# Performance work log

Hardware: AMD Instinct MI355X
Metric: run time of the kernel (lower is better)

## Reference

```python
import jax, jax.numpy as jnp
import numpy as np

T, N, NN = 16, 64, 32          # ob_T, agents, neighbors
D, H, DK, DFF, L = 512, 8, 64, 2048, 2
NUM_PRED, OB_R = 20, 2.0


def _w(k, shape):
    fan_in = shape[-2] if len(shape) > 1 else shape[-1]
    return jax.random.normal(k, shape, jnp.float32) / np.sqrt(fan_in).astype(np.float32)


def setup_inputs():
    key = jax.random.key(0)
    ks = jax.random.split(key, 16)
    return {
        "x": jax.random.normal(ks[0], (T, N, 6), jnp.float32),
        "neighbor": jax.random.normal(ks[1], (T, N, NN, 4), jnp.float32),
        "att_factor": jax.random.uniform(ks[2], (1,), jnp.float32),
        "Wx": _w(ks[3], (4, D)), "bx": jnp.zeros((D,), jnp.float32),
        "Wn": _w(ks[4], (3, D)), "bn": jnp.zeros((D,), jnp.float32),
        "Wpred": _w(ks[5], (D, 2)), "bpred": jnp.zeros((2,), jnp.float32),
        "WQ": _w(ks[6], (L, D, H * DK)),
        "WK": _w(ks[7], (L, D, H * DK)),
        "WV": _w(ks[8], (L, D, H * DK)),
        "Wfc": _w(ks[9], (L, H * DK, D)),
        "mha_ln_g": jnp.ones((L, D), jnp.float32), "mha_ln_b": jnp.zeros((L, D), jnp.float32),
        "WSI": _w(ks[10], (L, H * D, D)),
        "ffs_w1": _w(ks[11], (L, D, DFF)), "ffs_w2": _w(ks[12], (L, DFF, D)),
        "ffs_ln_g": jnp.ones((L, D), jnp.float32), "ffs_ln_b": jnp.zeros((L, D), jnp.float32),
        "ffi_w1": _w(ks[13], (L, D, DFF)), "ffi_w2": _w(ks[14], (L, DFF, D)),
        "ffi_ln_g": jnp.ones((L, D), jnp.float32), "ffi_ln_b": jnp.zeros((L, D), jnp.float32),
    }


def _ln(x, g, b, eps=1e-5):
    m = x.mean(-1, keepdims=True)
    v = x.var(-1, keepdims=True)
    return (x - m) / jnp.sqrt(v + eps) * g + b


def reference(x, neighbor, att_factor, Wx, bx, Wn, bn, Wpred, bpred,
              WQ, WK, WV, Wfc, mha_ln_g, mha_ln_b, WSI,
              ffs_w1, ffs_w2, ffs_ln_g, ffs_ln_b,
              ffi_w1, ffi_w2, ffi_ln_g, ffi_ln_b):
    # ---- trajectory features ----
    velocity = jnp.linalg.norm(x[:, :, 2:4], axis=-1, keepdims=True)
    v_angle = jnp.arctan(x[:, :, 5] / x[:, :, 4])[..., None]
    x_f = jnp.nan_to_num(jnp.concatenate([x[:, :, 0:2], velocity, v_angle], axis=-1))
    pos = x[..., :2]                                       # [T,N,2]
    v = jnp.concatenate([x[1:2, ..., 2:4], pos[1:] - pos[:-1]], axis=0)  # [T,N,2]
    dp = neighbor[..., :2] - pos[:, :, None, :]            # [T,N,Nn,2]
    dv = neighbor[..., 2:4] - v[:, :, None, :]
    dist = jnp.linalg.norm(dp, axis=-1)                    # [T,N,Nn]
    mask = (dist <= OB_R).transpose(1, 2, 0)               # [N,Nn,T] (query-time mask)
    dot_dp_v = jnp.einsum('tnmd,tnd->tnm', dp, v)
    bearing = dot_dp_v / (dist * jnp.linalg.norm(v, axis=-1)[:, :, None])
    bearing = jnp.where(jnp.isnan(bearing), 0.0, bearing)
    dot_dp_dv = jnp.einsum('tnmd,tnmd->tnm', dp, dv)
    tau = -dot_dp_dv / jnp.linalg.norm(dv, axis=-1)
    tau = jnp.clip(jnp.where(jnp.isnan(tau), 0.0, tau), 0.0, 7.0)
    mpd = jnp.linalg.norm(dp + tau[..., None] * dv, axis=-1)
    neighbor_f = jnp.nan_to_num(jnp.stack([dist, bearing, mpd], axis=-1))  # [T,N,Nn,3]

    # ---- positional encoding (note: pos * 10000^(2i/d), as in the source) ----
    position = jnp.arange(T, dtype=jnp.float32)[:, None]
    div = jnp.power(10000.0, jnp.arange(0, D, 2, dtype=jnp.float32) / D)
    pe = jnp.zeros((T, D), jnp.float32)
    pe = pe.at[:, 0::2].set(jnp.sin(position * div)).at[:, 1::2].set(jnp.cos(position * div))

    x_emb = (x_f @ Wx + bx) + pe[:, None, :]               # [T,N,D]
    n_emb = (neighbor_f @ Wn + bn) + pe[:, None, None, :]  # [T,N,Nn,D]
    x_emb = x_emb.transpose(1, 0, 2)                       # [N,T,D]
    n_emb = n_emb.transpose(1, 2, 0, 3)                    # [N,Nn,T,D]

    amask = mask[:, :, None, :, None]   # [N,Nn,1(heads),T(query),1(key)]
    factor = att_factor[0]
    sk = 1.0 / np.sqrt(DK).astype(np.float32)
    sd = 1.0 / np.sqrt(D).astype(np.float32)

    for l in range(L):
        # --- masked MHA over the time axis, per (agent, neighbor) ---
        q = (n_emb @ WQ[l]).reshape(N, NN, T, H, DK).transpose(0, 1, 3, 2, 4)
        k = (n_emb @ WK[l]).reshape(N, NN, T, H, DK).transpose(0, 1, 3, 2, 4)
        vv = (n_emb @ WV[l]).reshape(N, NN, T, H, DK).transpose(0, 1, 3, 2, 4)
        scores = jnp.einsum('bmhqd,bmhkd->bmhqk', q, k) * sk
        scores = jnp.where(amask, scores, -1e9)
        attn = jax.nn.softmax(scores, axis=-1)             # [N,Nn,H,T,T]
        ctx = jnp.einsum('bmhqk,bmhkd->bmhqd', attn, vv)
        ctx = ctx.transpose(0, 1, 3, 2, 4).reshape(N, NN, T, H * DK)
        res_inter = _ln(ctx @ Wfc[l] + n_emb, mha_ln_g[l], mha_ln_b[l])

        # --- self/inter attention fusion ---
        att_inter = attn.mean(axis=1)                      # [N,H,T,T]
        att_self = jax.nn.softmax(jnp.einsum('nqd,nkd->nqk', x_emb, x_emb) * sd, axis=-1)
        att = att_self[:, None, :, :] + factor * att_inter # [N,H,T,T]
        si = jnp.einsum('nhqt,ntd->nqhd', att, x_emb).reshape(N, T, H * D)
        x_new = si @ WSI[l]                                # [N,T,D]

        # --- FFN + LayerNorm (self and inter branches) ---
        x_emb = _ln(jax.nn.relu(x_new @ ffs_w1[l]) @ ffs_w2[l] + x_new,
                    ffs_ln_g[l], ffs_ln_b[l])
        n_emb = _ln(jax.nn.relu(res_inter @ ffi_w1[l]) @ ffi_w2[l] + res_inter,
                    ffi_ln_g[l], ffi_ln_b[l])

    out = x_emb @ Wpred + bpred                            # [N,T,2]
    out = jnp.broadcast_to(out[None], (NUM_PRED, N, T, 2)).transpose(0, 2, 1, 3)
    return out                                             # [20,T,N,2]
```

## Files before the change

### kernel.cpp

```cpp
#include <hip/hip_runtime.h>
#include <math.h>


#define T_ 16
#define N_ 64
#define NN_ 32
#define D_ 512
#define H_ 8
#define DK_ 64
#define DFF_ 2048
#define L_ 2
#define NPRED_ 20

typedef unsigned short u16;
typedef unsigned int u32;
typedef __attribute__((ext_vector_type(8))) short short8;
typedef __attribute__((ext_vector_type(4))) float f32x4;

__device__ __forceinline__ u16 f2bf(float f) {
    u32 u = __float_as_uint(f);
    u32 r = u + 0x7fffu + ((u >> 16) & 1u);
    return (u16)(r >> 16);
}
__device__ __forceinline__ float bfv(u16 v) {
    return __uint_as_float(((u32)v) << 16);
}
__device__ __forceinline__ float ntn(float v) {
    if (isnan(v)) return 0.0f;
    if (isinf(v)) return v > 0.0f ? 3.4028234663852886e38f : -3.4028234663852886e38f;
    return v;
}
__device__ __forceinline__ float wave_sum(float v) {
    #pragma unroll
    for (int o = 32; o > 0; o >>= 1) v += __shfl_xor(v, o, 64);
    return v;
}
__device__ __forceinline__ void gload_lds(const u16* g, u16* l) {
    __builtin_amdgcn_global_load_lds(
        (const __attribute__((address_space(1))) u32*)g,
        (__attribute__((address_space(3))) u32*)l, 16, 0, 0);
}

struct WJob { const float* src; u16* dst; int K; int N; int t0; };
struct WJobs { WJob j[14]; };
__global__ __launch_bounds__(256) void wconv_all(WJobs jobs, int ntiles) {
    int bid = blockIdx.x;
    if (bid >= ntiles) return;
    int ji = 0;
    #pragma unroll 1
    for (int i = 1; i < 14; ++i) if (bid >= jobs.j[i].t0) ji = i;
    const float* in = jobs.j[ji].src;
    u16* out = jobs.j[ji].dst;
    int K = jobs.j[ji].K, N = jobs.j[ji].N;
    int lt = bid - jobs.j[ji].t0;
    int ntx = N >> 5;
    int nb = (lt % ntx) * 32, kb = (lt / ntx) * 32;
    __shared__ float tile[32][33];
    int tx = threadIdx.x & 31, ty = threadIdx.x >> 5;
    #pragma unroll
    for (int r = ty; r < 32; r += 8)
        tile[r][tx] = in[(size_t)(kb + r) * N + nb + tx];
    __syncthreads();
    #pragma unroll
    for (int r = ty; r < 32; r += 8)
        out[(size_t)(nb + r) * K + kb + tx] = f2bf(tile[tx][r]);
}

template<int TM, int TN, int EPI, int WF32, int WBF16>
__global__ __launch_bounds__(256) void gemm_bt(
    const u16* __restrict__ Ab, const u16* __restrict__ Btb,
    float* __restrict__ Cf, u16* __restrict__ Cb, const void* __restrict__ Rg,
    int K, int ldc)
{
    constexpr int WR = TM / 32, WC = TN / 32;
    constexpr int ITA = TM / 32, ITB = TN / 32;
    __shared__ __align__(16) u16 As[TM][64];
    __shared__ __align__(16) u16 Bs[TN][64];
    int tid = threadIdx.x;
    int lane = tid & 63, wave = tid >> 6;
    int quad = lane >> 4, l16 = lane & 15;
    int wm = (wave >> 1) * (TM / 2), wn = (wave & 1) * (TN / 2);

    int gx = gridDim.x, gy = gridDim.y;
    int bx, by;
    if ((gy & 7) == 0) {
        int id = blockIdx.y * gx + blockIdx.x;
        int xcd = id & 7;
        int slot = id >> 3;
        bx = slot % gx;
        by = xcd * (gy >> 3) + slot / gx;
    } else {
        bx = blockIdx.x;
        by = blockIdx.y;
    }
    size_t row0 = (size_t)by * TM;
    size_t col0 = (size_t)bx * TN;

    f32x4 acc[WR][WC];
    #pragma unroll
    for (int i = 0; i < WR; ++i)
        #pragma unroll
        for (int j = 0; j < WC; ++j)
            acc[i][j] = (f32x4){0.f, 0.f, 0.f, 0.f};

    int srow = lane >> 3;
    int c8 = (lane & 7) ^ srow;
    int h8 = l16 & 7;

    for (int k0 = 0; k0 < K; k0 += 64) {
        __syncthreads();
        #pragma unroll
        for (int it = 0; it < ITA; ++it) {
            int g = wave + it * 4;
            gload_lds(Ab + (row0 + g * 8 + srow) * (size_t)K + k0 + c8 * 8, &As[g * 8][0]);
        }
        #pragma unroll
        for (int it = 0; it < ITB; ++it) {
            int g = wave + it * 4;
            gload_lds(Btb + (col0 + g * 8 + srow) * (size_t)K + k0 + c8 * 8, &Bs[g * 8][0]);
        }
        __syncthreads();
        #pragma unroll
        for (int s = 0; s < 2; ++s) {
            int coff = ((s * 4 + quad) ^ h8) * 8;
            short8 af[WR], bf[WC];
            #pragma unroll
            for (int i = 0; i < WR; ++i)
                af[i] = *(short8*)&As[wm + i * 16 + l16][coff];
            #pragma unroll
            for (int j = 0; j < WC; ++j)
                bf[j] = *(short8*)&Bs[wn + j * 16 + l16][coff];
            #pragma unroll
            for (int i = 0; i < WR; ++i)
                #pragma unroll
                for (int j = 0; j < WC; ++j)
                    acc[i][j] = __builtin_amdgcn_mfma_f32_16x16x32_bf16(
                        af[i], bf[j], acc[i][j], 0, 0, 0);
        }
    }
    #pragma unroll
    for (int i = 0; i < WR; ++i)
        #pragma unroll
        for (int j = 0; j < WC; ++j)
            #pragma unroll
            for (int reg = 0; reg < 4; ++reg) {
                size_t row = row0 + wm + i * 16 + quad * 4 + reg;
                size_t col = col0 + wn + j * 16 + l16;
                float v = acc[i][j][reg];
                if (EPI == 2) v += ((const float*)Rg)[row * (size_t)ldc + col];
                if (EPI == 3) v += bfv(((const u16*)Rg)[row * (size_t)ldc + col]);
                if (EPI == 1) v = fmaxf(v, 0.f);
                if (WF32)  Cf[row * (size_t)ldc + col] = v;
                if (WBF16) Cb[row * (size_t)ldc + col] = f2bf(v);
            }
}

template<int TM, int TN, int WMW, int WNW, int EPI, int WF32, int WBF16>
__global__ __launch_bounds__(WMW * WNW * 64, 2) void gemm_pp(
    const u16* __restrict__ Ab, const u16* __restrict__ Btb,
    float* __restrict__ Cf, u16* __restrict__ Cb, const void* __restrict__ Rg,
    int K, int ldc)
{
    constexpr int NW = WMW * WNW;
    constexpr int FM = TM / WMW / 16;
    constexpr int FN = TN / WNW / 16;
    constexpr int MH = (FM * FN > 16) ? 2 : 1;
    constexpr int FMp = FM / MH;
    constexpr int GA = TM / 8 / NW;
    constexpr int GB = TN / 8 / NW;
    __shared__ __align__(16) u16 As[2][TM][64];
    __shared__ __align__(16) u16 Bs[2][TN][64];
    int tid = threadIdx.x;
    int lane = tid & 63, wave = tid >> 6;
    int quad = lane >> 4, l16 = lane & 15;
    int wm = (wave / WNW) * (FM * 16);
    int wn = (wave % WNW) * (FN * 16);

    int gx = gridDim.x, gy = gridDim.y;
    int bx, by;
    {
        int id = blockIdx.y * gx + blockIdx.x;
        int xcd = id & 7, slot = id >> 3;
        bx = slot % gx;
        by = xcd * (gy >> 3) + slot / gx;
    }
    size_t row0 = (size_t)by * TM;
    size_t col0 = (size_t)bx * TN;

    f32x4 acc[FM][FN];
    #pragma unroll
    for (int i = 0; i < FM; ++i)
        #pragma unroll
        for (int j = 0; j < FN; ++j)
            acc[i][j] = (f32x4){0.f, 0.f, 0.f, 0.f};

    int srow = lane >> 3;
    int c8 = (lane & 7) ^ srow;
    int h8 = l16 & 7;
    size_t aoff[GA], boff[GB];
    #pragma unroll
    for (int it = 0; it < GA; ++it)
        aoff[it] = (row0 + (size_t)(wave + it * NW) * 8 + srow) * (size_t)K + c8 * 8;
    #pragma unroll
    for (int it = 0; it < GB; ++it)
        boff[it] = (col0 + (size_t)(wave + it * NW) * 8 + srow) * (size_t)K + c8 * 8;

    int nt = K >> 6;
    #pragma unroll
    for (int it = 0; it < GA; ++it)
        gload_lds(Ab + aoff[it], &As[0][(wave + it * NW) * 8][0]);
    #pragma unroll
    for (int it = 0; it < GB; ++it)
        gload_lds(Btb + boff[it], &Bs[0][(wave + it * NW) * 8][0]);
    asm volatile("s_waitcnt vmcnt(0)" ::: "memory");
    __builtin_amdgcn_s_barrier();

    #pragma unroll 1
    for (int t = 0; t < nt; ++t) {
        int cur = t & 1;
        if (t + 1 < nt) {
            size_t ko = (size_t)(t + 1) * 64;
            #pragma unroll
            for (int it = 0; it < GA; ++it)
                gload_lds(Ab + aoff[it] + ko, &As[cur ^ 1][(wave + it * NW) * 8][0]);
            #pragma unroll
            for (int it = 0; it < GB; ++it)
                gload_lds(Btb + boff[it] + ko, &Bs[cur ^ 1][(wave + it * NW) * 8][0]);
        }
        short8 bf[FN];
        #pragma unroll
        for (int kh = 0; kh < 2; ++kh) {
            #pragma unroll
            for (int mh = 0; mh < MH; ++mh) {
                int coff = ((kh * 4 + quad) ^ h8) * 8;
                short8 af[FMp];
                if (mh == 0) {
                    #pragma unroll
                    for (int j = 0; j < FN; ++j)
                        bf[j] = *(short8*)&Bs[cur][wn + j * 16 + l16][coff];
                }
                #pragma unroll
                for (int i = 0; i < FMp; ++i)
                    af[i] = *(short8*)&As[cur][wm + (mh * FMp + i) * 16 + l16][coff];
                __builtin_amdgcn_s_barrier();
                __builtin_amdgcn_s_setprio(1);
                #pragma unroll
                for (int i = 0; i < FMp; ++i)
                    #pragma unroll
                    for (int j = 0; j < FN; ++j)
                        acc[mh * FMp + i][j] = __builtin_amdgcn_mfma_f32_16x16x32_bf16(
                            af[i], bf[j], acc[mh * FMp + i][j], 0, 0, 0);
                __builtin_amdgcn_s_setprio(0);
                __builtin_amdgcn_s_barrier();
            }
        }
        if (t + 1 < nt)
            asm volatile("s_waitcnt vmcnt(0)" ::: "memory");
        __builtin_amdgcn_s_barrier();
    }

    #pragma unroll
    for (int i = 0; i < FM; ++i)
        #pragma unroll
        for (int j = 0; j < FN; ++j)
            #pragma unroll
            for (int reg = 0; reg < 4; ++reg) {
                size_t row = row0 + wm + i * 16 + quad * 4 + reg;
                size_t col = col0 + wn + j * 16 + l16;
                float v = acc[i][j][reg];
                if (EPI == 2) v += ((const float*)Rg)[row * (size_t)ldc + col];
                if (EPI == 3) v += bfv(((const u16*)Rg)[row * (size_t)ldc + col]);
                if (EPI == 1) v = fmaxf(v, 0.f);
                if (WF32)  Cf[row * (size_t)ldc + col] = v;
                if (WBF16) Cb[row * (size_t)ldc + col] = f2bf(v);
            }
}

template<int CTX, int LD>
__global__ __launch_bounds__(256) void attn_fused_kernel(
    const u16* __restrict__ QKVb, const float* __restrict__ maskf, int bm0,
    float* __restrict__ att_sum, u16* __restrict__ ctxb)
{
    __shared__ __align__(16) u16 sQ[16][520];
    __shared__ __align__(16) u16 sK[16][520];
    __shared__ __align__(16) u16 sV[CTX ? 16 : 1][520];
    __shared__ float s_p[H_][16][17];
    int bm_l = blockIdx.x;
    int tid = threadIdx.x;
    int t = tid >> 4, ch = (tid & 15) * 32;
    const u16* base = QKVb + ((size_t)bm_l * T_ + t) * LD;
    #pragma unroll
    for (int c = 0; c < 4; ++c) {
        *(uint4*)&sQ[t][ch + c * 8] = *(const uint4*)(base + ch + c * 8);
        *(uint4*)&sK[t][ch + c * 8] = *(const uint4*)(base + 512 + ch + c * 8);
        if (CTX) *(uint4*)&sV[t][ch + c * 8] = *(const uint4*)(base + 1024 + ch + c * 8);
    }
    __syncthreads();

    int b = (bm0 + bm_l) >> 5;

    #pragma unroll
    for (int r = 0; r < 8; ++r) {
        int h = r;
        int q = (tid >> 4) & 15, k = tid & 15;
        const u32* qu = (const u32*)&sQ[q][0] + h * 32;
        const u32* ku = (const u32*)&sK[k][0] + h * 32;
        float acc = 0.f;
        #pragma unroll
        for (int j = 0; j < 32; ++j) {
            u32 a = qu[j], bb = ku[j];
            acc += bfv((u16)(a & 0xffff)) * bfv((u16)(bb & 0xffff));
            acc += bfv((u16)(a >> 16))    * bfv((u16)(bb >> 16));
        }
        acc *= 0.125f;
        if (maskf[(size_t)(bm0 + bm_l) * T_ + q] == 0.0f) acc = -1e9f;
        s_p[h][q][k] = acc;
    }
    __syncthreads();
    if (tid < 128) {
        int h = tid >> 4, q = tid & 15;
        float mx = -3.4e38f;
        #pragma unroll
        for (int kk = 0; kk < 16; ++kk) mx = fmaxf(mx, s_p[h][q][kk]);
        float e[16], s = 0.f;
        #pragma unroll
        for (int kk = 0; kk < 16; ++kk) { e[kk] = expf(s_p[h][q][kk] - mx); s += e[kk]; }
        float inv = 1.0f / s;
        #pragma unroll
        for (int kk = 0; kk < 16; ++kk) s_p[h][q][kk] = e[kk] * inv;
    }
    __syncthreads();
    #pragma unroll
    for (int r = 0; r < 8; ++r) {
        int h = r;
        int q = (tid >> 4) & 15, k = tid & 15;
        atomicAdd(&att_sum[(((size_t)b * H_ + h) * T_ + q) * T_ + k], s_p[h][q][k]);
    }
    if (CTX) {
        #pragma unroll
        for (int rep = 0; rep < 16; ++rep) {
            int i2 = rep * 256 + tid;
            int tt = i2 >> 8, c2 = i2 & 255;
            int h = c2 >> 5;
            const float* pr = &s_p[h][tt][0];
            float a0 = 0.f, a1 = 0.f;
            #pragma unroll
            for (int kk = 0; kk < 16; ++kk) {
                u32 vv = *((const u32*)&sV[kk][0] + c2);
                float p = pr[kk];
                a0 += p * bfv((u16)(vv & 0xffff));
                a1 += p * bfv((u16)(vv >> 16));
            }
            u32 o = (u32)f2bf(a0) | ((u32)f2bf(a1) << 16);
            *((u32*)(ctxb + ((size_t)bm_l * T_ + tt) * D_) + c2) = o;
        }
    }
}

__global__ __launch_bounds__(256) void siatt_kernel(
    const float* __restrict__ xemb, const float* __restrict__ att_sum,
    const float* __restrict__ attf, u16* __restrict__ sib)
{
    __shared__ float sX[16][516];
    __shared__ float sS[16][17];
    __shared__ float sA[16][17];
    int n = blockIdx.x >> 3, h = blockIdx.x & 7;
    int tid = threadIdx.x;
    int t = tid >> 4, ch = (tid & 15) * 32;
    const float* src = xemb + ((size_t)n * T_ + t) * D_;
    #pragma unroll
    for (int c = 0; c < 8; ++c)
        *(float4*)&sX[t][ch + c * 4] = *(const float4*)(src + ch + c * 4);
    __syncthreads();
    int q = tid >> 4, k = tid & 15;
    {
        float acc = 0.f;
        for (int d = 0; d < D_; ++d) acc += sX[q][d] * sX[k][d];
        sS[q][k] = acc * 0.04419417382415922f;
    }
    __syncthreads();
    if (tid < T_) {
        float mx = -3.4e38f;
        #pragma unroll
        for (int kk = 0; kk < 16; ++kk) mx = fmaxf(mx, sS[tid][kk]);
        float e[16], s = 0.f;
        #pragma unroll
        for (int kk = 0; kk < 16; ++kk) { e[kk] = expf(sS[tid][kk] - mx); s += e[kk]; }
        float inv = 1.0f / s;
        #pragma unroll
        for (int kk = 0; kk < 16; ++kk) sS[tid][kk] = e[kk] * inv;
    }
    __syncthreads();
    float f = attf[0] * (1.0f / 32.0f);
    sA[q][k] = sS[q][k] + f * att_sum[((size_t)n * H_ + h) * 256 + q * 16 + k];
    __syncthreads();
    #pragma unroll
    for (int rep = 0; rep < 16; ++rep) {
        int i2 = rep * 256 + tid;
        int qq = i2 >> 8, d2 = (i2 & 255) * 2;
        const float* ar = &sA[qq][0];
        float a0 = 0.f, a1 = 0.f;
        #pragma unroll
        for (int tt = 0; tt < 16; ++tt) {
            float p = ar[tt];
            a0 += p * sX[tt][d2];
            a1 += p * sX[tt][d2 + 1];
        }
        u32 o = (u32)f2bf(a0) | ((u32)f2bf(a1) << 16);
        *((u32*)(sib + (size_t)n * T_ * 4096 + (size_t)qq * 4096 + h * 512) + (d2 >> 1)) = o;
    }
}

__global__ void pe_kernel(float* pe) {
    int i = blockIdx.x * blockDim.x + threadIdx.x;
    if (i >= T_ * 256) return;
    int t = i >> 8, j = i & 255;
    float dv = (float)pow(10000.0, (double)j / 256.0);
    float a = (float)t * dv;
    double ad = (double)a;
    pe[t * D_ + 2 * j]     = (float)sin(ad);
    pe[t * D_ + 2 * j + 1] = (float)cos(ad);
}

__global__ void xemb_kernel(const float* x, const float* Wx, const float* bx,
                            const float* pe, float* xemb) {
    int row = blockIdx.x;
    int t = row / N_, n = row % N_;
    float x0 = x[row * 6 + 0], x1 = x[row * 6 + 1];
    float x2 = x[row * 6 + 2], x3 = x[row * 6 + 3];
    float x4 = x[row * 6 + 4], x5 = x[row * 6 + 5];
    float vel = sqrtf(x2 * x2 + x3 * x3);
    float ang = atanf(x5 / x4);
    float f0 = ntn(x0), f1 = ntn(x1), f2 = ntn(vel), f3 = ntn(ang);
    for (int d = threadIdx.x; d < D_; d += blockDim.x) {
        xemb[((size_t)n * T_ + t) * D_ + d] =
            f0 * Wx[0 * D_ + d] + f1 * Wx[1 * D_ + d]
          + f2 * Wx[2 * D_ + d] + f3 * Wx[3 * D_ + d]
          + bx[d] + pe[t * D_ + d];
    }
}

__global__ void nbr_kernel(const float* x, const float* nbr, float* nf, float* maskf) {
    int idx = blockIdx.x * blockDim.x + threadIdx.x;
    if (idx >= T_ * N_ * NN_) return;
    int m = idx % NN_;
    int tn = idx / NN_;
    int n = tn % N_, t = tn / N_;
    float px = x[((size_t)t * N_ + n) * 6 + 0];
    float py = x[((size_t)t * N_ + n) * 6 + 1];
    float vx, vy;
    if (t == 0) {
        vx = x[((size_t)1 * N_ + n) * 6 + 2];
        vy = x[((size_t)1 * N_ + n) * 6 + 3];
    } else {
        vx = px - x[((size_t)(t - 1) * N_ + n) * 6 + 0];
        vy = py - x[((size_t)(t - 1) * N_ + n) * 6 + 1];
    }
    float nx  = nbr[(size_t)idx * 4 + 0], ny  = nbr[(size_t)idx * 4 + 1];
    float nvx = nbr[(size_t)idx * 4 + 2], nvy = nbr[(size_t)idx * 4 + 3];
    float dpx = nx - px, dpy = ny - py;
    float dvx = nvx - vx, dvy = nvy - vy;
    float dist = sqrtf(dpx * dpx + dpy * dpy);
    maskf[((size_t)n * NN_ + m) * T_ + t] = (dist <= 2.0f) ? 1.0f : 0.0f;
    float vn = sqrtf(vx * vx + vy * vy);
    float bearing = (dpx * vx + dpy * vy) / (dist * vn);
    if (isnan(bearing)) bearing = 0.0f;
    float dvn = sqrtf(dvx * dvx + dvy * dvy);
    float tau = -(dpx * dvx + dpy * dvy) / dvn;
    if (isnan(tau)) tau = 0.0f;
    tau = fminf(fmaxf(tau, 0.0f), 7.0f);
    float mx_ = dpx + tau * dvx, my_ = dpy + tau * dvy;
    float mpd = sqrtf(mx_ * mx_ + my_ * my_);
    nf[(size_t)idx * 3 + 0] = ntn(dist);
    nf[(size_t)idx * 3 + 1] = ntn(bearing);
    nf[(size_t)idx * 3 + 2] = ntn(mpd);
}

__global__ void nemb_kernel(const float* nf, const float* Wn, const float* bn,
                            const float* pe, u16* Ab) {
    int row = blockIdx.x;
    int t = row % T_;
    int bm = row / T_;
    int m = bm % NN_, b = bm / NN_;
    size_t nfrow = (((size_t)t * N_ + b) * NN_ + m) * 3;
    float f0 = nf[nfrow], f1 = nf[nfrow + 1], f2 = nf[nfrow + 2];
    for (int d = threadIdx.x; d < D_; d += blockDim.x) {
        float v = f0 * Wn[d] + f1 * Wn[D_ + d] + f2 * Wn[2 * D_ + d]
                + bn[d] + pe[t * D_ + d];
        Ab[(size_t)row * D_ + d] = f2bf(v);
    }
}

template<int INBF>
__global__ __launch_bounds__(256) void ln_kernel(
    const void* X, const float* g, const float* b, float* outF, u16* outB, int nrows) {
    int row = blockIdx.x * 4 + (threadIdx.x >> 6);
    if (row >= nrows) return;
    int lane = threadIdx.x & 63;
    float v[8];
    float s = 0.f;
    #pragma unroll
    for (int r = 0; r < 8; ++r) {
        int d = lane + r * 64;
        v[r] = INBF ? bfv(((const u16*)X)[(size_t)row * D_ + d])
                    : ((const float*)X)[(size_t)row * D_ + d];
        s += v[r];
    }
    s = wave_sum(s);
    float mean = s * (1.0f / 512.0f);
    float vs = 0.f;
    #pragma unroll
    for (int r = 0; r < 8; ++r) { float d = v[r] - mean; vs += d * d; }
    vs = wave_sum(vs);
    float rstd = rsqrtf(vs * (1.0f / 512.0f) + 1e-5f);
    #pragma unroll
    for (int r = 0; r < 8; ++r) {
        int d = lane + r * 64;
        float o = (v[r] - mean) * rstd * g[d] + b[d];
        if (outF) outF[(size_t)row * D_ + d] = o;
        if (outB) outB[(size_t)row * D_ + d] = f2bf(o);
    }
}

__global__ void predbcast_kernel(const float* xemb, const float* Wp, const float* bp,
                                 float* out) {
    int idx = blockIdx.x * blockDim.x + threadIdx.x;
    if (idx >= N_ * T_ * 2) return;
    int c = idx & 1;
    int nt = idx >> 1;
    int n = nt / T_, t = nt % T_;
    float acc = bp[c];
    for (int j = 0; j < D_; ++j) acc += xemb[(size_t)nt * D_ + j] * Wp[(size_t)j * 2 + c];
    #pragma unroll
    for (int p = 0; p < NPRED_; ++p)
        out[(((size_t)p * T_ + t) * N_ + n) * 2 + c] = acc;
}

extern "C" void kernel_launch(void* const* d_in, const int* in_sizes, int n_in,
                              void* d_out, int out_size, void* d_ws, size_t ws_size,
                              hipStream_t stream) {
    (void)in_sizes; (void)n_in; (void)out_size; (void)ws_size;

    const float* x    = (const float*)d_in[0];
    const float* nbr  = (const float*)d_in[1];
    const float* attf = (const float*)d_in[2];
    const float* Wx   = (const float*)d_in[3];
    const float* bx   = (const float*)d_in[4];
    const float* Wn   = (const float*)d_in[5];
    const float* bn   = (const float*)d_in[6];
    const float* Wp   = (const float*)d_in[7];
    const float* bp   = (const float*)d_in[8];
    const float* WQ   = (const float*)d_in[9];
    const float* WK   = (const float*)d_in[10];
    const float* WV   = (const float*)d_in[11];
    const float* Wfc  = (const float*)d_in[12];
    const float* mlng = (const float*)d_in[13];
    const float* mlnb = (const float*)d_in[14];
    const float* WSI  = (const float*)d_in[15];
    const float* fsw1 = (const float*)d_in[16];
    const float* fsw2 = (const float*)d_in[17];
    const float* fsg  = (const float*)d_in[18];
    const float* fsb  = (const float*)d_in[19];
    const float* fiw1 = (const float*)d_in[20];
    const float* fiw2 = (const float*)d_in[21];
    const float* fig  = (const float*)d_in[22];
    const float* fib  = (const float*)d_in[23];

    char* w = (char*)d_ws;
    size_t off = 0;
    auto alloc = [&](size_t bytes) -> void* {
        void* p = w + off;
        off = (off + bytes + 255) & ~(size_t)255;
        return p;
    };
    const size_t MiB = 1024 * 1024;

    const int BM = N_ * NN_;
    const int ROWS_I = BM * T_;
    const int CB = 1024;
    const int RC = CB * T_;
    const int NCH = ROWS_I / RC;

    float* pe      = (float*)alloc((size_t)T_ * D_ * 4);
    float* xemb    = (float*)alloc((size_t)N_ * T_ * D_ * 4);
    float* nf      = (float*)alloc((size_t)T_ * N_ * NN_ * 3 * 4);
    float* maskf   = (float*)alloc((size_t)BM * T_ * 4);
    u16*   Ab      = (u16*)alloc((size_t)ROWS_I * D_ * 2);
    u16* tQKV[2], *tWSI[2], *tfs1[2], *tfs2[2];
    for (int l = 0; l < 2; ++l) {
        tQKV[l] = (u16*)alloc((size_t)1536 * 512 * 2);
        tWSI[l] = (u16*)alloc((size_t)512 * 4096 * 2);
        tfs1[l] = (u16*)alloc((size_t)2048 * 512 * 2);
        tfs2[l] = (u16*)alloc((size_t)512 * 2048 * 2);
    }
    u16* tWfc = (u16*)alloc((size_t)512 * 512 * 2);
    u16* tfi1 = (u16*)alloc((size_t)2048 * 512 * 2);
    u16* tfi2 = (u16*)alloc((size_t)512 * 2048 * 2);
    char* SCR  = (char*)alloc(64 * MiB);
    u16*   QKVb = (u16*)SCR;
    u16*   ctxb = (u16*)(SCR + 48 * MiB);
    u16*   hid  = (u16*)SCR;
    u16*   BbA    = (u16*)alloc((size_t)RC * D_ * 2);
    u16*   Bb_res = (u16*)alloc((size_t)RC * D_ * 2);
    float* att_sum = (float*)alloc((size_t)N_ * H_ * 256 * 4);
    u16*   sib     = (u16*)alloc((size_t)N_ * T_ * 4096 * 2);
    float* xnew    = (float*)alloc((size_t)N_ * T_ * D_ * 4);
    u16*   xnb     = (u16*)alloc((size_t)N_ * T_ * D_ * 2);

    WJobs jobs;
    int ntiles = 0;
    auto addJob = [&](int idx, const float* src, u16* dst, int K, int N) {
        jobs.j[idx] = {src, dst, K, N, ntiles};
        ntiles += (N >> 5) * (K >> 5);
    };
    addJob(0,  WQ,                            tQKV[0],              512, 512);
    addJob(1,  WK,                            tQKV[0] + 512 * 512,  512, 512);
    addJob(2,  WV,                            tQKV[0] + 1024 * 512, 512, 512);
    addJob(3,  WQ + (size_t)512 * 512,        tQKV[1],              512, 512);
    addJob(4,  WK + (size_t)512 * 512,        tQKV[1] + 512 * 512,  512, 512);
    addJob(5,  Wfc,                           tWfc,                 512, 512);
    addJob(6,  WSI,                           tWSI[0],              4096, 512);
    addJob(7,  WSI + (size_t)4096 * 512,      tWSI[1],              4096, 512);
    addJob(8,  fsw1,                          tfs1[0],              512, 2048);
    addJob(9,  fsw1 + (size_t)512 * 2048,     tfs1[1],              512, 2048);
    addJob(10, fsw2,                          tfs2[0],              2048, 512);
    addJob(11, fsw2 + (size_t)2048 * 512,     tfs2[1],              2048, 512);
    addJob(12, fiw1,                          tfi1,                 512, 2048);
    addJob(13, fiw2,                          tfi2,                 2048, 512);
    wconv_all<<<ntiles, 256, 0, stream>>>(jobs, ntiles);

    pe_kernel<<<16, 256, 0, stream>>>(pe);
    xemb_kernel<<<T_ * N_, 256, 0, stream>>>(x, Wx, bx, pe, xemb);
    nbr_kernel<<<(T_ * N_ * NN_ + 255) / 256, 256, 0, stream>>>(x, nbr, nf, maskf);
    nemb_kernel<<<BM * T_, 256, 0, stream>>>(nf, Wn, bn, pe, Ab);

    for (int l = 0; l < L_; ++l) {
        hipMemsetAsync(att_sum, 0, (size_t)N_ * H_ * 256 * 4, stream);
        if (l == 0) {
            for (int c = 0; c < NCH; ++c) {
                u16* Acb = Ab + (size_t)c * RC * D_;
                gemm_pp<128, 128, 2, 2, 0, 0, 1><<<dim3(12, RC / 128), 256, 0, stream>>>(
                    Acb, tQKV[0], nullptr, QKVb, nullptr, 512, 1536);
                attn_fused_kernel<1, 1536><<<CB, 256, 0, stream>>>(
                    QKVb, maskf, c * CB, att_sum, ctxb);
                gemm_pp<128, 128, 2, 2, 3, 0, 1><<<dim3(4, RC / 128), 256, 0, stream>>>(
                    ctxb, tWfc, nullptr, BbA, Acb, 512, 512);
                ln_kernel<1><<<RC / 4, 256, 0, stream>>>(
                    BbA, mlng, mlnb, nullptr, Bb_res, RC);
                gemm_pp<256, 256, 2, 4, 1, 0, 1><<<dim3(8, RC / 256), 512, 0, stream>>>(
                    Bb_res, tfi1, nullptr, hid, nullptr, 512, 2048);
                gemm_pp<128, 128, 2, 2, 3, 0, 1><<<dim3(4, RC / 128), 256, 0, stream>>>(
                    hid, tfi2, nullptr, BbA, Bb_res, 2048, 512);
                ln_kernel<1><<<RC / 4, 256, 0, stream>>>(
                    BbA, fig, fib, nullptr, Acb, RC);
            }
        } else {
            gemm_pp<256, 256, 2, 4, 0, 0, 1><<<dim3(4, ROWS_I / 256), 512, 0, stream>>>(
                Ab, tQKV[1], nullptr, QKVb, nullptr, 512, 1024);
            attn_fused_kernel<0, 1024><<<BM, 256, 0, stream>>>(
                QKVb, maskf, 0, att_sum, nullptr);
        }

        siatt_kernel<<<N_ * H_, 256, 0, stream>>>(xemb, att_sum, attf, sib);
        gemm_bt<32, 64, 0, 1, 1><<<dim3(8, 32), 256, 0, stream>>>(
            sib, tWSI[l], xnew, xnb, nullptr, 4096, 512);
        gemm_bt<32, 64, 1, 0, 1><<<dim3(32, 32), 256, 0, stream>>>(
            xnb, tfs1[l], nullptr, hid, nullptr, 512, 2048);
        gemm_bt<32, 64, 2, 1, 0><<<dim3(8, 32), 256, 0, stream>>>(
            hid, tfs2[l], xemb, nullptr, xnew, 2048, 512);
        ln_kernel<0><<<(N_ * T_) / 4, 256, 0, stream>>>(
            xemb, fsg + l * D_, fsb + l * D_, xemb, nullptr, N_ * T_);
    }

    predbcast_kernel<<<(N_ * T_ * 2 + 255) / 256, 256, 0, stream>>>(
        xemb, Wp, bp, (float*)d_out);
}
```

Before: 840.4 us.

## Rework bf16 GEMM pipeline with partial vmcnt waits and larger 512-thread tiles

Replaces gemm_pp with gemm_cp. The new kernel waits only for the current K-tile's global-to-LDS loads (partial vmcnt) rather than draining all outstanding loads, and it drops the inner per-half barriers so each wave loads all A/B fragments and issues its MFMAs in one batch. The 128x128 four-wave launches become 256x128 eight-wave launches. The goal is to overlap prefetch with compute and cut barrier count, at the cost of more registers per wave and fewer blocks per launch. The 256x256 tile uses FM*FN=32 accumulators with no split, which raises register pressure.

```diff
diff --git a/kernel.cpp b/kernel.cpp
--- a/kernel.cpp
+++ b/kernel.cpp
@@ -155,17 +155,15 @@
             }
 }
 
-template<int TM, int TN, int WMW, int WNW, int EPI, int WF32, int WBF16>
-__global__ __launch_bounds__(WMW * WNW * 64, 2) void gemm_pp(
+template<int TM, int TN, int WM, int WN, int EPI, int WF32, int WBF16>
+__global__ __launch_bounds__(512, 2) void gemm_cp(
     const u16* __restrict__ Ab, const u16* __restrict__ Btb,
     float* __restrict__ Cf, u16* __restrict__ Cb, const void* __restrict__ Rg,
     int K, int ldc)
 {
-    constexpr int NW = WMW * WNW;
-    constexpr int FM = TM / WMW / 16;
-    constexpr int FN = TN / WNW / 16;
-    constexpr int MH = (FM * FN > 16) ? 2 : 1;
-    constexpr int FMp = FM / MH;
+    constexpr int NW = WM * WN;
+    constexpr int FM = TM / WM / 16;
+    constexpr int FN = TN / WN / 16;
     constexpr int GA = TM / 8 / NW;
     constexpr int GB = TN / 8 / NW;
     __shared__ __align__(16) u16 As[2][TM][64];
@@ -173,17 +171,14 @@
     int tid = threadIdx.x;
     int lane = tid & 63, wave = tid >> 6;
     int quad = lane >> 4, l16 = lane & 15;
-    int wm = (wave / WNW) * (FM * 16);
-    int wn = (wave % WNW) * (FN * 16);
+    int wm = (wave / WN) * (FM * 16);
+    int wn = (wave % WN) * (FN * 16);
 
     int gx = gridDim.x, gy = gridDim.y;
-    int bx, by;
-    {
-        int id = blockIdx.y * gx + blockIdx.x;
-        int xcd = id & 7, slot = id >> 3;
-        bx = slot % gx;
-        by = xcd * (gy >> 3) + slot / gx;
-    }
+    int id = blockIdx.y * gx + blockIdx.x;
+    int xcd = id & 7, slot = id >> 3;
+    int bx = slot % gx;
+    int by = xcd * (gy >> 3) + slot / gx;
     size_t row0 = (size_t)by * TM;
     size_t col0 = (size_t)bx * TN;
 
@@ -212,8 +207,6 @@
     #pragma unroll
     for (int it = 0; it < GB; ++it)
         gload_lds(Btb + boff[it], &Bs[0][(wave + it * NW) * 8][0]);
-    asm volatile("s_waitcnt vmcnt(0)" ::: "memory");
-    __builtin_amdgcn_s_barrier();
 
     #pragma unroll 1
     for (int t = 0; t < nt; ++t) {
@@ -226,36 +219,40 @@
             #pragma unroll
             for (int it = 0; it < GB; ++it)
                 gload_lds(Btb + boff[it] + ko, &Bs[cur ^ 1][(wave + it * NW) * 8][0]);
-        }
-        short8 bf[FN];
+            __builtin_amdgcn_sched_barrier(0);
+            if constexpr (GA + GB == 8)
+                asm volatile("s_waitcnt vmcnt(8)" ::: "memory");
+            else if constexpr (GA + GB == 6)
+                asm volatile("s_waitcnt vmcnt(6)" ::: "memory");
+            else
+                asm volatile("s_waitcnt vmcnt(4)" ::: "memory");
+        } else {
+            __builtin_amdgcn_sched_barrier(0);
+            asm volatile("s_waitcnt vmcnt(0)" ::: "memory");
+        }
+        __builtin_amdgcn_sched_barrier(0);
+        __builtin_amdgcn_s_barrier();
+        __builtin_amdgcn_sched_barrier(0);
+        __builtin_amdgcn_s_setprio(1);
         #pragma unroll
         for (int kh = 0; kh < 2; ++kh) {
-            #pragma unroll
-            for (int mh = 0; mh < MH; ++mh) {
-                int coff = ((kh * 4 + quad) ^ h8) * 8;
-                short8 af[FMp];
-                if (mh == 0) {
-                    #pragma unroll
-                    for (int j = 0; j < FN; ++j)
-                        bf[j] = *(short8*)&Bs[cur][wn + j * 16 + l16][coff];
-                }
+            int coff = ((kh * 4 + quad) ^ h8) * 8;
+            short8 af[FM], bf[FN];
+            #pragma unroll
+            for (int j = 0; j < FN; ++j)
+                bf[j] = *(short8*)&Bs[cur][wn + j * 16 + l16][coff];
+            #pragma unroll
+            for (int i = 0; i < FM; ++i)
+                af[i] = *(short8*)&As[cur][wm + i * 16 + l16][coff];
+            #pragma unroll
+            for (int i = 0; i < FM; ++i)
                 #pragma unroll
-                for (int i = 0; i < FMp; ++i)
-                    af[i] = *(short8*)&As[cur][wm + (mh * FMp + i) * 16 + l16][coff];
-                __builtin_amdgcn_s_barrier();
-                __builtin_amdgcn_s_setprio(1);
-                #pragma unroll
-                for (int i = 0; i < FMp; ++i)
-                    #pragma unroll
-                    for (int j = 0; j < FN; ++j)
-                        acc[mh * FMp + i][j] = __builtin_amdgcn_mfma_f32_16x16x32_bf16(
-                            af[i], bf[j], acc[mh * FMp + i][j], 0, 0, 0);
-                __builtin_amdgcn_s_setprio(0);
-                __builtin_amdgcn_s_barrier();
-            }
-        }
-        if (t + 1 < nt)
-            asm volatile("s_waitcnt vmcnt(0)" ::: "memory");
+                for (int j = 0; j < FN; ++j)
+                    acc[i][j] = __builtin_amdgcn_mfma_f32_16x16x32_bf16(
+                        af[i], bf[j], acc[i][j], 0, 0, 0);
+        }
+        __builtin_amdgcn_s_setprio(0);
+        __builtin_amdgcn_sched_barrier(0);
         __builtin_amdgcn_s_barrier();
     }
 
@@ -639,23 +636,23 @@
         if (l == 0) {
             for (int c = 0; c < NCH; ++c) {
                 u16* Acb = Ab + (size_t)c * RC * D_;
-                gemm_pp<128, 128, 2, 2, 0, 0, 1><<<dim3(12, RC / 128), 256, 0, stream>>>(
+                gemm_cp<256, 128, 4, 2, 0, 0, 1><<<dim3(12, RC / 256), 512, 0, stream>>>(
                     Acb, tQKV[0], nullptr, QKVb, nullptr, 512, 1536);
                 attn_fused_kernel<1, 1536><<<CB, 256, 0, stream>>>(
                     QKVb, maskf, c * CB, att_sum, ctxb);
-                gemm_pp<128, 128, 2, 2, 3, 0, 1><<<dim3(4, RC / 128), 256, 0, stream>>>(
+                gemm_cp<256, 128, 4, 2, 3, 0, 1><<<dim3(4, RC / 256), 512, 0, stream>>>(
                     ctxb, tWfc, nullptr, BbA, Acb, 512, 512);
                 ln_kernel<1><<<RC / 4, 256, 0, stream>>>(
                     BbA, mlng, mlnb, nullptr, Bb_res, RC);
-                gemm_pp<256, 256, 2, 4, 1, 0, 1><<<dim3(8, RC / 256), 512, 0, stream>>>(
+                gemm_cp<256, 256, 2, 4, 1, 0, 1><<<dim3(8, RC / 256), 512, 0, stream>>>(
                     Bb_res, tfi1, nullptr, hid, nullptr, 512, 2048);
-                gemm_pp<128, 128, 2, 2, 3, 0, 1><<<dim3(4, RC / 128), 256, 0, stream>>>(
+                gemm_cp<256, 128, 4, 2, 3, 0, 1><<<dim3(4, RC / 256), 512, 0, stream>>>(
                     hid, tfi2, nullptr, BbA, Bb_res, 2048, 512);
                 ln_kernel<1><<<RC / 4, 256, 0, stream>>>(
                     BbA, fig, fib, nullptr, Acb, RC);
             }
         } else {
-            gemm_pp<256, 256, 2, 4, 0, 0, 1><<<dim3(4, ROWS_I / 256), 512, 0, stream>>>(
+            gemm_cp<256, 256, 2, 4, 0, 0, 1><<<dim3(4, ROWS_I / 256), 512, 0, stream>>>(
                 Ab, tQKV[1], nullptr, QKVb, nullptr, 512, 1024);
             attn_fused_kernel<0, 1024><<<BM, 256, 0, stream>>>(
                 QKVb, maskf, 0, att_sum, nullptr);
```

Measured after the change: 854.5 us. No clear change (+1.7%).
